# Performance work log

Measured on AMD Instinct MI355X. Metric: run time of the kernel, lower is better.

## Reference

```python
import jax, jax.numpy as jnp
import numpy as np

B, T, C = 16, 2048, 384
HEAD = 384

def setup_inputs() -> dict:
    key = jax.random.key(0)
    kx, kq, kk, kv = jax.random.split(key, 4)
    s = 1.0 / np.sqrt(C)
    return {
        "x": jax.random.normal(kx, (B, T, C), dtype=jnp.float32),
        "Wq": jax.random.normal(kq, (C, HEAD), dtype=jnp.float32) * s,
        "Wk": jax.random.normal(kk, (C, HEAD), dtype=jnp.float32) * s,
        "Wv": jax.random.normal(kv, (C, HEAD), dtype=jnp.float32) * s,
    }

def reference(x, Wq, Wk, Wv):
    # x: [B,T,C]; single causal attention head, eval mode (dropout = identity)
    Bc, Tc, Cc = x.shape
    q = jnp.einsum('btc,ch->bth', x, Wq)
    k = jnp.einsum('btc,ch->bth', x, Wk)
    v = jnp.einsum('btc,ch->bth', x, Wv)
    # NOTE: original scales by C**-0.5 (embedding dim), not head_size**-0.5
    scale = Cc ** (-0.5)
    wei = jnp.einsum('bth,bsh->bts', q, k) * scale  # [B,T,T]
    causal = jnp.tril(jnp.ones((Tc, Tc), dtype=bool))
    wei = jnp.where(causal, wei, -jnp.inf)
    wei = jax.nn.softmax(wei, axis=-1)
    out = jnp.einsum('bts,bsh->bth', wei, v)  # [B,T,head]
    return out
```

## Files before the change

kernel.cpp:

```cpp
#include <hip/hip_runtime.h>
#include <hip/hip_bf16.h>

#define NB 16
#define TT 2048
#define CC 384

typedef short bf16x8 __attribute__((ext_vector_type(8)));
typedef float f32x4 __attribute__((ext_vector_type(4)));

static __device__ __forceinline__ short f2bf(float f) {
  union { __hip_bfloat16 h; short s; } u;
  u.h = __float2bfloat16(f);
  return u.s;
}

#define QSC (0.051031036307982884f * 1.4426950408889634f)

__global__ __launch_bounds__(384)
void conv_wt(const float* __restrict__ Wq, const float* __restrict__ Wk,
             const float* __restrict__ Wv, short* __restrict__ Wbt) {
  const int w = blockIdx.x / CC;
  const int n = blockIdx.x % CC;
  const int k = threadIdx.x;
  const float* W = (w == 0) ? Wq : (w == 1) ? Wk : Wv;
  Wbt[((size_t)w * CC + n) * CC + k] = f2bf(W[(size_t)k * CC + n]);
}

__global__ __launch_bounds__(256)
void xconv(const float* __restrict__ x, short* __restrict__ xb) {
  const int i = (blockIdx.x * 256 + threadIdx.x) * 8;
  const float4 a = *(const float4*)(x + i);
  const float4 c = *(const float4*)(x + i + 4);
  bf16x8 r;
  r[0] = f2bf(a.x); r[1] = f2bf(a.y); r[2] = f2bf(a.z); r[3] = f2bf(a.w);
  r[4] = f2bf(c.x); r[5] = f2bf(c.y); r[6] = f2bf(c.z); r[7] = f2bf(c.w);
  *(bf16x8*)(xb + i) = r;
}

__global__ __launch_bounds__(256, 2)
void proj_gemm(const short* __restrict__ xb, const short* __restrict__ Wbt,
               short* __restrict__ Q, short* __restrict__ K,
               short* __restrict__ Vt) {
  __shared__ char smem[65536];
  short* Es = (short*)smem;

  const int mt = blockIdx.x & 255;
  const int nt = blockIdx.x >> 8;
  const int wsel = nt / 3;
  const int nc0 = (nt % 3) * 128;
  const int tid = threadIdx.x;
  const int wave = tid >> 6, lane = tid & 63;
  const int l15 = lane & 15, quad = lane >> 4;
  const int wm = (wave & 1) * 64, wn = (wave >> 1) * 64;

  const short* Ab = xb + (size_t)mt * 128 * CC;
  const short* Bb = Wbt + ((size_t)wsel * CC + nc0) * CC;

  int aoff[4];
  #pragma unroll
  for (int j = 0; j < 4; ++j) {
    const int lin = wave * 4096 + j * 1024 + lane * 16;
    const int r = lin >> 7;
    const int s = (lin >> 4) & 7;
    aoff[j] = r * CC + ((s ^ (r & 7)) << 3);
  }

  f32x4 acc[16];
  #pragma unroll
  for (int i = 0; i < 16; ++i) acc[i] = f32x4{0.f, 0.f, 0.f, 0.f};

  #pragma unroll
  for (int pc = 0; pc < 2; ++pc) {
    #pragma unroll
    for (int j = 0; j < 4; ++j)
      __builtin_amdgcn_global_load_lds(
          (const __attribute__((address_space(1))) void*)(Ab + pc * 64 + aoff[j]),
          (__attribute__((address_space(3))) void*)(smem + pc * 16384 + wave * 4096 + j * 1024), 16, 0, 0);
    #pragma unroll
    for (int j = 0; j < 4; ++j)
      __builtin_amdgcn_global_load_lds(
          (const __attribute__((address_space(1))) void*)(Bb + pc * 64 + aoff[j]),
          (__attribute__((address_space(3))) void*)(smem + 32768 + pc * 16384 + wave * 4096 + j * 1024), 16, 0, 0);
  }

  for (int kt = 0; kt < 6; ++kt) {
    const int kb = kt & 1;
    if (kt == 5) {
      asm volatile("s_waitcnt vmcnt(0)" ::: "memory");
    } else {
      asm volatile("s_waitcnt vmcnt(8)" ::: "memory");
    }
    __builtin_amdgcn_s_barrier();
    __builtin_amdgcn_sched_barrier(0);

    const char* As = smem + kb * 16384;
    const char* Bs = smem + 32768 + kb * 16384;
    #pragma unroll
    for (int ks = 0; ks < 2; ++ks) {
      bf16x8 af[4], bf[4];
      #pragma unroll
      for (int i = 0; i < 4; ++i) {
        const int ar = wm + i * 16 + l15;
        const int br = wn + i * 16 + l15;
        af[i] = *(const bf16x8*)(As + ar * 128 + (((ks * 4 + quad) ^ (ar & 7)) << 4));
        bf[i] = *(const bf16x8*)(Bs + br * 128 + (((ks * 4 + quad) ^ (br & 7)) << 4));
      }
      #pragma unroll
      for (int i = 0; i < 4; ++i)
        #pragma unroll
        for (int j = 0; j < 4; ++j)
          acc[i * 4 + j] =
              __builtin_amdgcn_mfma_f32_16x16x32_bf16(af[i], bf[j], acc[i * 4 + j], 0, 0, 0);
    }

    __builtin_amdgcn_sched_barrier(0);
    __builtin_amdgcn_s_barrier();
    if (kt + 2 < 6) {
      const int k0 = (kt + 2) * 64;
      #pragma unroll
      for (int j = 0; j < 4; ++j)
        __builtin_amdgcn_global_load_lds(
            (const __attribute__((address_space(1))) void*)(Ab + k0 + aoff[j]),
            (__attribute__((address_space(3))) void*)(smem + kb * 16384 + wave * 4096 + j * 1024), 16, 0, 0);
      #pragma unroll
      for (int j = 0; j < 4; ++j)
        __builtin_amdgcn_global_load_lds(
            (const __attribute__((address_space(1))) void*)(Bb + k0 + aoff[j]),
            (__attribute__((address_space(3))) void*)(smem + 32768 + kb * 16384 + wave * 4096 + j * 1024), 16, 0, 0);
    }
  }

  if (nt < 6) {
    short* O = (nt < 3) ? Q : K;
    const float sc = (nt < 3) ? QSC : 1.0f;
    #pragma unroll
    for (int i = 0; i < 4; ++i)
      #pragma unroll
      for (int j = 0; j < 4; ++j) {
        const f32x4 a = acc[i * 4 + j];
        const int r0 = mt * 128 + wm + i * 16 + quad * 4;
        const int c = nc0 + wn + j * 16 + l15;
        #pragma unroll
        for (int r = 0; r < 4; ++r) O[(size_t)(r0 + r) * CC + c] = f2bf(a[r] * sc);
      }
  } else {
    __syncthreads();
    #pragma unroll
    for (int i = 0; i < 4; ++i)
      #pragma unroll
      for (int j = 0; j < 4; ++j) {
        const f32x4 a = acc[i * 4 + j];
        const int dl = wn + j * 16 + l15;
        const int ml = wm + i * 16 + quad * 4;
        short4 p4;
        p4.x = f2bf(a[0]); p4.y = f2bf(a[1]); p4.z = f2bf(a[2]); p4.w = f2bf(a[3]);
        *(short4*)(Es + (size_t)dl * 136 + ml) = p4;
      }
    __syncthreads();
    const int d0 = (nt - 6) * 128;
    const int b = mt >> 4, t0 = (mt & 15) * 128;
    const int dr = tid >> 1, hf = tid & 1;
    const short* src = Es + (size_t)dr * 136 + hf * 64;
    short* dst = Vt + ((size_t)b * CC + d0 + dr) * TT + t0 + hf * 64;
    #pragma unroll
    for (int c = 0; c < 8; ++c)
      *(bf16x8*)(dst + c * 8) = *(const bf16x8*)(src + c * 8);
  }
}


#define ATTN_PRELUDE                                                          \
  __shared__ char sm[54272];                                                  \
  char* KsS = sm;                                                             \
  char* VsS = sm + 24576;                                                     \
  const int tid = threadIdx.x;                                                \
  const int wave = tid >> 6, lane = tid & 63;                                 \
  const int l15 = lane & 15, quad = lane >> 4;                                \
  short* pw = (short*)(sm + 49152) + wave * 640;                              \
  bf16x8 onesf;                                                               \
  _Pragma("unroll")                                                           \
  for (int i = 0; i < 8; ++i) onesf[i] = (short)0x3F80;                       \
  int koff[6], voff[6];                                                       \
  _Pragma("unroll")                                                           \
  for (int j = 0; j < 6; ++j) {                                               \
    const int lin = wave * 6144 + j * 1024 + lane * 16;                       \
    const int kr = lin / 768;                                                 \
    const int ksl = (lin - kr * 768) >> 4;                                    \
    koff[j] = kr * 768 + ((ksl ^ (kr & 7)) << 4);                             \
    const int vr = lin >> 6;                                                  \
    const int vsl = (lin >> 4) & 3;                                           \
    voff[j] = vr * 4096 + (((vsl - (vr >> 2)) & 3) << 4);                     \
  }                                                                           \
  char* KsW = KsS + wave * 6144;                                              \
  char* VsW = VsS + wave * 6144;

#define STAGE_K(ck)                                                           \
  do {                                                                        \
    const size_t kby_ = (size_t)(ck) * 24576;                                 \
    _Pragma("unroll")                                                         \
    for (int j5 = 0; j5 < 6; ++j5)                                            \
      __builtin_amdgcn_global_load_lds(                                       \
          (const __attribute__((address_space(1))) void*)(kbB + kby_ + koff[j5]), \
          (__attribute__((address_space(3))) void*)(KsW + j5 * 1024), 16, 0, 0);  \
  } while (0)

#define STAGE_V(ck)                                                           \
  do {                                                                        \
    const size_t vby_ = (size_t)(ck) * 64;                                    \
    _Pragma("unroll")                                                         \
    for (int j5 = 0; j5 < 6; ++j5)                                            \
      __builtin_amdgcn_global_load_lds(                                       \
          (const __attribute__((address_space(1))) void*)(vtB + vby_ + voff[j5]), \
          (__attribute__((address_space(3))) void*)(VsW + j5 * 1024), 16, 0, 0);  \
  } while (0)

__global__ __launch_bounds__(256, 2)
void attn_plain(const short* __restrict__ Q, const short* __restrict__ K,
                const short* __restrict__ Vt, float* __restrict__ out) {
  ATTN_PRELUDE
  const int blk = blockIdx.x;
  const int qt = 31 - (blk >> 4);
  const int b  = blk & 15;
  const int q0 = qt * 64 + wave * 16;

  bf16x8 qf[12];
  const short* qp = Q + ((size_t)b * TT + q0 + l15) * CC + quad * 8;
  #pragma unroll
  for (int ks = 0; ks < 12; ++ks) qf[ks] = *(const bf16x8*)(qp + ks * 32);

  f32x4 o[24];
  #pragma unroll
  for (int n = 0; n < 24; ++n) o[n] = f32x4{0.f, 0.f, 0.f, 0.f};
  f32x4 lsum = f32x4{0.f, 0.f, 0.f, 0.f};
  float m[4];
  #pragma unroll
  for (int r = 0; r < 4; ++r) m[r] = -INFINITY;

  const char* kbB = (const char*)(K + (size_t)b * TT * CC);
  const char* vtB = (const char*)(Vt + (size_t)b * CC * TT);
  const int nchunk = qt * 2 + 2;

  STAGE_K(0);
  STAGE_V(0);

  for (int kc = 0; kc < nchunk; ++kc) {
    const int k0 = kc * 32;
    asm volatile("s_waitcnt vmcnt(6)" ::: "memory");
    __builtin_amdgcn_s_barrier();
    __builtin_amdgcn_sched_barrier(0);

    f32x4 s0 = f32x4{0.f, 0.f, 0.f, 0.f};
    f32x4 s1 = f32x4{0.f, 0.f, 0.f, 0.f};
    const bool active = (k0 <= q0 + 15);
    if (active) {
      #pragma unroll
      for (int ks = 0; ks < 12; ++ks) {
        const int sl = (ks * 4 + quad) ^ (l15 & 7);
        const bf16x8 b0 = *(const bf16x8*)(KsS + l15 * 768 + (sl << 4));
        const bf16x8 b1 = *(const bf16x8*)(KsS + (16 + l15) * 768 + (sl << 4));
        s0 = __builtin_amdgcn_mfma_f32_16x16x32_bf16(qf[ks], b0, s0, 0, 0, 0);
        s1 = __builtin_amdgcn_mfma_f32_16x16x32_bf16(qf[ks], b1, s1, 0, 0, 0);
      }
    }
    __builtin_amdgcn_sched_barrier(0);
    __builtin_amdgcn_s_barrier();
    { const int kn = (kc + 1 < nchunk) ? (kc + 1) : kc; STAGE_K(kn); }
    asm volatile("s_waitcnt vmcnt(6)" ::: "memory");
    __builtin_amdgcn_s_barrier();
    __builtin_amdgcn_sched_barrier(0);

    if (active) {
      const bool domask = (k0 + 31 > q0);
      float mx[4];
      #pragma unroll
      for (int r = 0; r < 4; ++r) {
        float a = s0[r], c = s1[r];
        if (domask) {
          const int qg = q0 + quad * 4 + r;
          if (k0 + l15 > qg)      a = -INFINITY;
          if (k0 + 16 + l15 > qg) c = -INFINITY;
        }
        s0[r] = a; s1[r] = c;
        float v = fmaxf(a, c);
        v = fmaxf(v, __shfl_xor(v, 1));
        v = fmaxf(v, __shfl_xor(v, 2));
        v = fmaxf(v, __shfl_xor(v, 4));
        v = fmaxf(v, __shfl_xor(v, 8));
        mx[r] = v;
      }
      float alpha[4];
      #pragma unroll
      for (int r = 0; r < 4; ++r) {
        const float mn = fmaxf(m[r], mx[r]);
        alpha[r] = exp2f(m[r] - mn);
        m[r] = mn;
        s0[r] = exp2f(s0[r] - mn);
        s1[r] = exp2f(s1[r] - mn);
      }
      const bool need = (alpha[0] < 1.f) | (alpha[1] < 1.f) |
                        (alpha[2] < 1.f) | (alpha[3] < 1.f);
      if (__any(need)) {
        #pragma unroll
        for (int r = 0; r < 4; ++r) lsum[r] *= alpha[r];
        #pragma unroll
        for (int n = 0; n < 24; ++n) {
          #pragma unroll
          for (int r = 0; r < 4; ++r) o[n][r] *= alpha[r];
        }
      }
      #pragma unroll
      for (int r = 0; r < 4; ++r) {
        pw[(quad * 4 + r) * 40 + l15]      = f2bf(s0[r]);
        pw[(quad * 4 + r) * 40 + 16 + l15] = f2bf(s1[r]);
      }
      const bf16x8 pf = *(const bf16x8*)(pw + l15 * 40 + quad * 8);
      lsum = __builtin_amdgcn_mfma_f32_16x16x32_bf16(pf, onesf, lsum, 0, 0, 0);
      #pragma unroll
      for (int n = 0; n < 24; ++n) {
        const int vrow = n * 16 + l15;
        const bf16x8 vf = *(const bf16x8*)(VsS + vrow * 64 + (((quad + (vrow >> 2)) & 3) << 4));
        o[n] = __builtin_amdgcn_mfma_f32_16x16x32_bf16(pf, vf, o[n], 0, 0, 0);
      }
    }
    __builtin_amdgcn_sched_barrier(0);
    __builtin_amdgcn_s_barrier();
    { const int kn = (kc + 1 < nchunk) ? (kc + 1) : kc; STAGE_V(kn); }
  }

  float linv[4];
  #pragma unroll
  for (int r = 0; r < 4; ++r) linv[r] = 1.f / lsum[r];
  float* ob = out + ((size_t)b * TT + q0) * CC;
  #pragma unroll
  for (int n = 0; n < 24; ++n) {
    #pragma unroll
    for (int r = 0; r < 4; ++r) {
      ob[(size_t)(quad * 4 + r) * CC + n * 16 + l15] = o[n][r] * linv[r];
    }
  }
}

__global__ __launch_bounds__(256, 2)
void attn_split(const short* __restrict__ Q, const short* __restrict__ K,
                const short* __restrict__ Vt, float* __restrict__ out,
                float* __restrict__ OB, float* __restrict__ ML) {
  ATTN_PRELUDE
  const int blk = blockIdx.x;
  const int b = blk & 15;
  const int s = blk >> 4;
  const int j = s & 15;
  const int role = s >> 4;

  const char* kbB = (const char*)(K + (size_t)b * TT * CC);
  const char* vtB = (const char*)(Vt + (size_t)b * CC * TT);

  #pragma unroll 1
  for (int ph = 0; ph < 2; ++ph) {
    const int qt = ph ? j : (31 - j);
    const int tile = b * 32 + qt;
    const int nchunk = qt * 2 + 2;
    const int q0 = qt * 64 + wave * 16;

    bf16x8 qf[12];
    const short* qp = Q + ((size_t)b * TT + q0 + l15) * CC + quad * 8;
    #pragma unroll
    for (int ks = 0; ks < 12; ++ks) qf[ks] = *(const bf16x8*)(qp + ks * 32);
    asm volatile("s_waitcnt vmcnt(0)" ::: "memory");

    f32x4 o[24];
    #pragma unroll
    for (int n = 0; n < 24; ++n) o[n] = f32x4{0.f, 0.f, 0.f, 0.f};
    f32x4 lsum = f32x4{0.f, 0.f, 0.f, 0.f};
    float m[4];
    #pragma unroll
    for (int r = 0; r < 4; ++r) m[r] = -INFINITY;

    STAGE_K(role);
    STAGE_V(role);

    #pragma unroll 1
    for (int kc = role; kc < nchunk; kc += 2) {
      const int k0 = kc * 32;
      asm volatile("s_waitcnt vmcnt(6)" ::: "memory");
      __builtin_amdgcn_s_barrier();
      __builtin_amdgcn_sched_barrier(0);

      f32x4 s0 = f32x4{0.f, 0.f, 0.f, 0.f};
      f32x4 s1 = f32x4{0.f, 0.f, 0.f, 0.f};
      const bool active = (k0 <= q0 + 15);
      if (active) {
        #pragma unroll
        for (int ks = 0; ks < 12; ++ks) {
          const int sl = (ks * 4 + quad) ^ (l15 & 7);
          const bf16x8 b0 = *(const bf16x8*)(KsS + l15 * 768 + (sl << 4));
          const bf16x8 b1 = *(const bf16x8*)(KsS + (16 + l15) * 768 + (sl << 4));
          s0 = __builtin_amdgcn_mfma_f32_16x16x32_bf16(qf[ks], b0, s0, 0, 0, 0);
          s1 = __builtin_amdgcn_mfma_f32_16x16x32_bf16(qf[ks], b1, s1, 0, 0, 0);
        }
      }
      __builtin_amdgcn_sched_barrier(0);
      __builtin_amdgcn_s_barrier();
      { const int kn = (kc + 2 < nchunk) ? (kc + 2) : kc; STAGE_K(kn); }
      asm volatile("s_waitcnt vmcnt(6)" ::: "memory");
      __builtin_amdgcn_s_barrier();
      __builtin_amdgcn_sched_barrier(0);

      if (active) {
        const bool domask = (k0 + 31 > q0);
        float mx[4];
        #pragma unroll
        for (int r = 0; r < 4; ++r) {
          float a = s0[r], c = s1[r];
          if (domask) {
            const int qg = q0 + quad * 4 + r;
            if (k0 + l15 > qg)      a = -INFINITY;
            if (k0 + 16 + l15 > qg) c = -INFINITY;
          }
          s0[r] = a; s1[r] = c;
          float v = fmaxf(a, c);
          v = fmaxf(v, __shfl_xor(v, 1));
          v = fmaxf(v, __shfl_xor(v, 2));
          v = fmaxf(v, __shfl_xor(v, 4));
          v = fmaxf(v, __shfl_xor(v, 8));
          mx[r] = v;
        }
        float alpha[4];
        #pragma unroll
        for (int r = 0; r < 4; ++r) {
          const float mn = fmaxf(m[r], mx[r]);
          alpha[r] = exp2f(m[r] - mn);
          m[r] = mn;
          s0[r] = exp2f(s0[r] - mn);
          s1[r] = exp2f(s1[r] - mn);
        }
        const bool need = (alpha[0] < 1.f) | (alpha[1] < 1.f) |
                          (alpha[2] < 1.f) | (alpha[3] < 1.f);
        if (__any(need)) {
          #pragma unroll
          for (int r = 0; r < 4; ++r) lsum[r] *= alpha[r];
          #pragma unroll
          for (int n = 0; n < 24; ++n) {
            #pragma unroll
            for (int r = 0; r < 4; ++r) o[n][r] *= alpha[r];
          }
        }
        #pragma unroll
        for (int r = 0; r < 4; ++r) {
          pw[(quad * 4 + r) * 40 + l15]      = f2bf(s0[r]);
          pw[(quad * 4 + r) * 40 + 16 + l15] = f2bf(s1[r]);
        }
        const bf16x8 pf = *(const bf16x8*)(pw + l15 * 40 + quad * 8);
        lsum = __builtin_amdgcn_mfma_f32_16x16x32_bf16(pf, onesf, lsum, 0, 0, 0);
        #pragma unroll
        for (int n = 0; n < 24; ++n) {
          const int vrow = n * 16 + l15;
          const bf16x8 vf = *(const bf16x8*)(VsS + vrow * 64 + (((quad + (vrow >> 2)) & 3) << 4));
          o[n] = __builtin_amdgcn_mfma_f32_16x16x32_bf16(pf, vf, o[n], 0, 0, 0);
        }
      }
      __builtin_amdgcn_sched_barrier(0);
      __builtin_amdgcn_s_barrier();
      { const int kn = (kc + 2 < nchunk) ? (kc + 2) : kc; STAGE_V(kn); }
    }

    float* ob = (role == 0)
        ? out + ((size_t)b * TT + q0) * CC
        : OB + (size_t)tile * 24576 + (size_t)(wave * 16) * CC;
    #pragma unroll
    for (int n = 0; n < 24; ++n) {
      #pragma unroll
      for (int r = 0; r < 4; ++r)
        ob[(size_t)(quad * 4 + r) * CC + n * 16 + l15] = o[n][r];
    }
    if (l15 == 0) {
      float* pml = ML + (size_t)tile * 256 + role * 128;
      #pragma unroll
      for (int r = 0; r < 4; ++r) {
        pml[(wave * 16 + quad * 4 + r) * 2]     = m[r];
        pml[(wave * 16 + quad * 4 + r) * 2 + 1] = lsum[r];
      }
    }
  }
}

__global__ __launch_bounds__(256)
void combine(float* __restrict__ out, const float* __restrict__ OB,
             const float* __restrict__ ML) {
  const int t = blockIdx.x;
  const int b = t >> 5, qt = t & 31;
  const int row = threadIdx.x >> 2, seg = threadIdx.x & 3;
  const float* ml = ML + (size_t)t * 256;
  const float mA = ml[row * 2],       lA = ml[row * 2 + 1];
  const float mB = ml[128 + row * 2], lB = ml[128 + row * 2 + 1];
  const float mF = fmaxf(mA, mB);
  const float sA = exp2f(mA - mF), sB = exp2f(mB - mF);
  const float inv = 1.f / (lA * sA + lB * sB);
  const float wA = sA * inv, wB = sB * inv;
  float* pa = out + ((size_t)b * TT + qt * 64 + row) * CC + seg * 96;
  const float* pb = OB + (size_t)t * 24576 + (size_t)row * CC + seg * 96;
  #pragma unroll
  for (int c = 0; c < 24; ++c) {
    float4 a = *(float4*)(pa + c * 4);
    const float4 bb = *(const float4*)(pb + c * 4);
    a.x = a.x * wA + bb.x * wB;
    a.y = a.y * wA + bb.y * wB;
    a.z = a.z * wA + bb.z * wB;
    a.w = a.w * wA + bb.w * wB;
    *(float4*)(pa + c * 4) = a;
  }
}

extern "C" void kernel_launch(void* const* d_in, const int* in_sizes, int n_in,
                              void* d_out, int out_size, void* d_ws, size_t ws_size,
                              hipStream_t stream) {
  const float* x  = (const float*)d_in[0];
  const float* Wq = (const float*)d_in[1];
  const float* Wk = (const float*)d_in[2];
  const float* Wv = (const float*)d_in[3];
  float* out = (float*)d_out;

  const size_t QS = (size_t)NB * TT * CC;
  short* Qs = (short*)d_ws;
  short* Ks = Qs + QS;
  short* Vt = Ks + QS;

  const size_t base = QS * 3 * 2;
  float* OB = (float*)((char*)d_ws + base);
  float* ML = (float*)((char*)d_ws + base + 50331648);
  const bool split = ws_size >= base + 50331648 + 524288;

  short* Wbt = (short*)d_out;
  short* xb  = (short*)((char*)d_out + 1048576);

  hipLaunchKernelGGL(conv_wt, dim3(3 * CC), dim3(CC), 0, stream, Wq, Wk, Wv, Wbt);
  hipLaunchKernelGGL(xconv, dim3(6144), dim3(256), 0, stream, x, xb);
  hipLaunchKernelGGL(proj_gemm, dim3(256 * 9), dim3(256), 0, stream,
                     xb, Wbt, Qs, Ks, Vt);
  if (split) {
    hipLaunchKernelGGL(attn_split, dim3(512), dim3(256), 0, stream,
                       Qs, Ks, Vt, out, OB, ML);
    hipLaunchKernelGGL(combine, dim3(512), dim3(256), 0, stream, out, OB, ML);
  } else {
    hipLaunchKernelGGL(attn_plain, dim3(512), dim3(256), 0, stream,
                       Qs, Ks, Vt, out);
  }
}
```

Measured before the change: 341.3 us.

## Rebalance causal attention split so only the long query tile is split

Changes the work partition in the split attention kernel. Role-0 blocks now fully compute the short query tile j, normalizing it directly, and then handle part of the long tile 31-j. Role-1 blocks process the rest of the long tile with 33 chunks. Only one tile per pair needs combining, which halves the partial-output buffer and the combine grid. This is meant to cut partial-result write/read traffic and combine work while keeping per-block work balanced, at the cost of a more complex chunk-index schedule.

```diff
diff --git a/kernel.cpp b/kernel.cpp
--- a/kernel.cpp
+++ b/kernel.cpp
@@ -350,15 +350,19 @@
   const int s = blk >> 4;
   const int j = s & 15;
   const int role = s >> 4;
+  const int p = b * 16 + j;
 
   const char* kbB = (const char*)(K + (size_t)b * TT * CC);
   const char* vtB = (const char*)(Vt + (size_t)b * CC * TT);
 
+  const int nph = role ? 1 : 2;
   #pragma unroll 1
-  for (int ph = 0; ph < 2; ++ph) {
-    const int qt = ph ? j : (31 - j);
-    const int tile = b * 32 + qt;
-    const int nchunk = qt * 2 + 2;
+  for (int ph = 0; ph < nph; ++ph) {
+    int qt, count, pivot, base, mode;
+    if (role == 0) {
+      if (ph == 0) { qt = j;      count = 2 * j + 2;  pivot = 64;        base = 0;         mode = 0; }
+      else         { qt = 31 - j; count = 31 - 2 * j; pivot = 0;         base = 2 * j + 2; mode = 1; }
+    } else         { qt = 31 - j; count = 33;         pivot = 2 * j + 2; base = 2 * j + 3; mode = 2; }
     const int q0 = qt * 64 + wave * 16;
 
     bf16x8 qf[12];
@@ -375,11 +379,15 @@
     #pragma unroll
     for (int r = 0; r < 4; ++r) m[r] = -INFINITY;
 
-    STAGE_K(role);
-    STAGE_V(role);
+    const int ck0 = (0 < pivot) ? 0 : base;
+    STAGE_K(ck0);
+    STAGE_V(ck0);
 
     #pragma unroll 1
-    for (int kc = role; kc < nchunk; kc += 2) {
+    for (int i = 0; i < count; ++i) {
+      const int kc = (i < pivot) ? i : (base + 2 * (i - pivot));
+      const int in = (i + 1 < count) ? (i + 1) : i;
+      const int kn = (in < pivot) ? in : (base + 2 * (in - pivot));
       const int k0 = kc * 32;
       asm volatile("s_waitcnt vmcnt(6)" ::: "memory");
       __builtin_amdgcn_s_barrier();
@@ -400,7 +408,7 @@
       }
       __builtin_amdgcn_sched_barrier(0);
       __builtin_amdgcn_s_barrier();
-      { const int kn = (kc + 2 < nchunk) ? (kc + 2) : kc; STAGE_K(kn); }
+      STAGE_K(kn);
       asm volatile("s_waitcnt vmcnt(6)" ::: "memory");
       __builtin_amdgcn_s_barrier();
       __builtin_amdgcn_sched_barrier(0);
@@ -460,24 +468,37 @@
       }
       __builtin_amdgcn_sched_barrier(0);
       __builtin_amdgcn_s_barrier();
-      { const int kn = (kc + 2 < nchunk) ? (kc + 2) : kc; STAGE_V(kn); }
-    }
-
-    float* ob = (role == 0)
-        ? out + ((size_t)b * TT + q0) * CC
-        : OB + (size_t)tile * 24576 + (size_t)(wave * 16) * CC;
-    #pragma unroll
-    for (int n = 0; n < 24; ++n) {
-      #pragma unroll
-      for (int r = 0; r < 4; ++r)
-        ob[(size_t)(quad * 4 + r) * CC + n * 16 + l15] = o[n][r];
-    }
-    if (l15 == 0) {
-      float* pml = ML + (size_t)tile * 256 + role * 128;
-      #pragma unroll
-      for (int r = 0; r < 4; ++r) {
-        pml[(wave * 16 + quad * 4 + r) * 2]     = m[r];
-        pml[(wave * 16 + quad * 4 + r) * 2 + 1] = lsum[r];
+      STAGE_V(kn);
+    }
+
+    if (mode == 0) {
+      float linv[4];
+      #pragma unroll
+      for (int r = 0; r < 4; ++r) linv[r] = 1.f / lsum[r];
+      float* ob = out + ((size_t)b * TT + q0) * CC;
+      #pragma unroll
+      for (int n = 0; n < 24; ++n) {
+        #pragma unroll
+        for (int r = 0; r < 4; ++r)
+          ob[(size_t)(quad * 4 + r) * CC + n * 16 + l15] = o[n][r] * linv[r];
+      }
+    } else {
+      float* ob = (mode == 2)
+          ? out + ((size_t)b * TT + q0) * CC
+          : OB + (size_t)p * 24576 + (size_t)(wave * 16) * CC;
+      #pragma unroll
+      for (int n = 0; n < 24; ++n) {
+        #pragma unroll
+        for (int r = 0; r < 4; ++r)
+          ob[(size_t)(quad * 4 + r) * CC + n * 16 + l15] = o[n][r];
+      }
+      if (l15 == 0) {
+        float* pml = ML + (size_t)p * 256 + ((mode == 2) ? 0 : 128);
+        #pragma unroll
+        for (int r = 0; r < 4; ++r) {
+          pml[(wave * 16 + quad * 4 + r) * 2]     = m[r];
+          pml[(wave * 16 + quad * 4 + r) * 2 + 1] = lsum[r];
+        }
       }
     }
   }
@@ -486,18 +507,19 @@
 __global__ __launch_bounds__(256)
 void combine(float* __restrict__ out, const float* __restrict__ OB,
              const float* __restrict__ ML) {
-  const int t = blockIdx.x;
-  const int b = t >> 5, qt = t & 31;
+  const int p = blockIdx.x;
+  const int b = p >> 4, j = p & 15;
+  const int H = 31 - j;
   const int row = threadIdx.x >> 2, seg = threadIdx.x & 3;
-  const float* ml = ML + (size_t)t * 256;
+  const float* ml = ML + (size_t)p * 256;
   const float mA = ml[row * 2],       lA = ml[row * 2 + 1];
   const float mB = ml[128 + row * 2], lB = ml[128 + row * 2 + 1];
   const float mF = fmaxf(mA, mB);
   const float sA = exp2f(mA - mF), sB = exp2f(mB - mF);
   const float inv = 1.f / (lA * sA + lB * sB);
   const float wA = sA * inv, wB = sB * inv;
-  float* pa = out + ((size_t)b * TT + qt * 64 + row) * CC + seg * 96;
-  const float* pb = OB + (size_t)t * 24576 + (size_t)row * CC + seg * 96;
+  float* pa = out + ((size_t)b * TT + H * 64 + row) * CC + seg * 96;
+  const float* pb = OB + (size_t)p * 24576 + (size_t)row * CC + seg * 96;
   #pragma unroll
   for (int c = 0; c < 24; ++c) {
     float4 a = *(float4*)(pa + c * 4);
@@ -526,8 +548,8 @@
 
   const size_t base = QS * 3 * 2;
   float* OB = (float*)((char*)d_ws + base);
-  float* ML = (float*)((char*)d_ws + base + 50331648);
-  const bool split = ws_size >= base + 50331648 + 524288;
+  float* ML = (float*)((char*)d_ws + base + 25165824);
+  const bool split = ws_size >= base + 25165824 + 262144;
 
   short* Wbt = (short*)d_out;
   short* xb  = (short*)((char*)d_out + 1048576);
@@ -539,7 +561,7 @@
   if (split) {
     hipLaunchKernelGGL(attn_split, dim3(512), dim3(256), 0, stream,
                        Qs, Ks, Vt, out, OB, ML);
-    hipLaunchKernelGGL(combine, dim3(512), dim3(256), 0, stream, out, OB, ML);
+    hipLaunchKernelGGL(combine, dim3(256), dim3(256), 0, stream, out, OB, ML);
   } else {
     hipLaunchKernelGGL(attn_plain, dim3(512), dim3(256), 0, stream,
                        Qs, Ks, Vt, out);
```

Result: faster. 303.7 us (-11.0%).
